# Optimization experiments

Measured on AMD Instinct MI355X. Metric: run time of the kernel, lower is better.

The kernel has to match this reference:

```python
import jax, jax.numpy as jnp
import numpy as np

B, TXT_T, MEL_T, N_MEL = 32, 256, 1600, 40
PAD_MAG = 1.0e12


def setup_inputs() -> dict:
    key = jax.random.key(0)
    k1, k2, k3, k4 = jax.random.split(key, 4)
    mu_logvar = jax.random.normal(k1, (B, TXT_T, 2 * N_MEL), jnp.float32)
    z = jax.random.normal(k2, (B, N_MEL, MEL_T), jnp.float32)
    text_lengths = jax.random.randint(k3, (B,), TXT_T // 2, TXT_T + 1).astype(jnp.int32)
    mel_lengths = jax.random.randint(k4, (B,), MEL_T // 2, MEL_T + 1).astype(jnp.int32)
    return {"mu_logvar": mu_logvar, "z": z,
            "text_lengths": text_lengths, "mel_lengths": mel_lengths}


def _mdn_log_prob(mu_logvar, z):
    # mu_logvar: [B, L, 2C], z: [B, C, T] -> log_prob_matrix [B, L, T]
    C = z.shape[1]
    mu, logvar = jnp.split(mu_logvar, 2, axis=-1)          # [B, L, C] each
    invvar = jnp.exp(-logvar)                               # [B, L, C]
    # mean_c((z - mu)^2 * invvar) expanded via matmuls (no [B,L,T,C] tensor)
    t1 = jnp.einsum('bct,blc->blt', z * z, invvar)
    t2 = jnp.einsum('bct,blc->blt', z, mu * invvar)
    t3 = jnp.sum(mu * mu * invvar, axis=-1)[:, :, None]
    mse = t1 - 2.0 * t2 + t3                                # [B, L, T]
    return -0.5 * (mse / C + jnp.mean(logvar, axis=-1)[:, :, None])


def _forward_dp(lp):
    # forward algorithm: log_alpha over (txt position, mel time) via scan over T
    Bb, L, T = lp.shape
    alpha0 = jnp.full((Bb, L + 1), -PAD_MAG, lp.dtype).at[:, 1].set(lp[:, 0, 0])

    def step(alpha, lp_t):
        stay = alpha[:, 1:] + 1e-7
        go = alpha[:, :-1] + 1e-7
        new = jnp.logaddexp(stay, go) + lp_t                # [B, L]
        alpha_new = jnp.concatenate(
            [jnp.full((Bb, 1), -PAD_MAG, lp.dtype), new], axis=1)
        return alpha_new, new

    _, ys = jax.lax.scan(step, alpha0, jnp.moveaxis(lp[:, :, 1:], 2, 0))
    log_alpha = jnp.concatenate([alpha0[:, 1:][None], ys], axis=0)  # [T, B, L]
    return log_alpha


def _viterbi(lp, text_lengths, mel_lengths):
    Bb, L, T = lp.shape
    beta0 = jnp.full((Bb, L), -PAD_MAG, lp.dtype).at[:, 0].set(lp[:, 0, 0])

    def fstep(beta, lp_t):
        shifted = jnp.concatenate(
            [jnp.full((Bb, 1), -PAD_MAG, lp.dtype), beta[:, :-1]], axis=1)
        new = jnp.maximum(beta, shifted) + lp_t
        return new, new

    _, ys = jax.lax.scan(fstep, beta0, jnp.moveaxis(lp[:, :, 1:], 2, 0))
    log_beta = jnp.transpose(jnp.concatenate([beta0[None], ys], axis=0), (1, 2, 0))  # [B, L, T]

    b_idx = jnp.arange(Bb)
    r0 = (text_lengths - 1).astype(jnp.float32)
    c0 = (mel_lengths - 1).astype(jnp.float32)

    def bstep(carry, _):
        rows, cols = carry
        ri = rows.astype(jnp.int32)
        ci = cols.astype(jnp.int32)
        # torch negative indexing wraps -> emulate with mod
        val_go = log_beta[b_idx, (ri - 1) % L, (ci - 1) % T]
        val_stay = log_beta[b_idx, ri % L, (ci - 1) % T]
        is_go = (val_go > val_stay).astype(rows.dtype)
        new_rows = jax.nn.relu(rows - is_go + 1.0) - 1.0
        new_cols = jax.nn.relu(cols) - 1.0
        return (new_rows, new_cols), new_rows

    _, path_ys = jax.lax.scan(bstep, (r0, c0), None, length=T - 1)
    full = jnp.concatenate([r0[None], path_ys], axis=0)     # [T, B], backward order
    path = full[::-1].T                                     # [B, T], chronological
    align = jax.nn.one_hot(path.astype(jnp.int32), L, dtype=lp.dtype)  # [B, T, L]

    def shift(a, ml):
        # F.pad(..., (-pad, pad)) on time axis: shift valid region to the front
        rolled = jnp.roll(a, -(T - ml), axis=0)
        mask = (jnp.arange(T) < ml)[:, None].astype(a.dtype)
        return rolled * mask

    return jax.vmap(shift)(align, mel_lengths)              # [B, T, L]


def reference(mu_logvar, z, text_lengths, mel_lengths):
    lp = _mdn_log_prob(mu_logvar, z)                        # [B, L, T]
    log_alpha = _forward_dp(lp)                             # [T, B, L]
    b_idx = jnp.arange(lp.shape[0])
    alpha_last = log_alpha[mel_lengths - 1, b_idx, text_lengths - 1]
    mdn_loss = -(alpha_last / mel_lengths.astype(alpha_last.dtype))  # [B]
    alignment = _viterbi(lp, text_lengths, mel_lengths)     # [B, T, L]
    return mdn_loss, alignment, lp
```

## Files before the change

### kernel.cpp

```cpp
#include <hip/hip_runtime.h>
#include <cstdint>
#include <math.h>

#define BB   32
#define LLEN 256
#define TLEN 1600
#define NC   40
#define NEGPADF (-1.0e12f)
#define NEGPADD (-1.0e12)

#define LOG2E_F 1.4426950408889634f
#define LN2_F   0.6931471805599453f
#define C7F     1.4426950408889634e-7f
#define PA_F 1.4426950f
#define PB_F (-0.6484000f)
#define PC_F 0.2057000f

#define OFF_ALIGN 32
#define OFF_LP    (32 + (size_t)BB * TLEN * LLEN)

#define WSB_A    0
#define WSB_KC   (WSB_A + (size_t)BB * LLEN * 80 * 8)
#define WSB_LPT  (WSB_KC + (size_t)BB * LLEN * 8)

__device__ __forceinline__ int imin(int a, int b) { return a < b ? a : b; }

#define WAIT_LGKM0 0xC07F
#define WAIT_VM0   0x3F70

__device__ __forceinline__ int rot1_i32(int x) {
  return __builtin_amdgcn_mov_dpp(x, 0x13C , 0xF, 0xF, true);
}
__device__ __forceinline__ float rot1_f32(float x) {
  return __int_as_float(rot1_i32(__float_as_int(x)));
}
__device__ __forceinline__ double rot1_f64(double x) {
  long long v = __double_as_longlong(x);
  int lo = rot1_i32((int)(v & 0xffffffffLL));
  int hi = rot1_i32((int)(v >> 32));
  return __longlong_as_double(((long long)hi << 32) | (unsigned long long)(unsigned int)lo);
}

__global__ __launch_bounds__(256) void prep_kernel(
    const float* __restrict__ mu_logvar, double* __restrict__ A, double* __restrict__ Kc) {
  int row = blockIdx.x * 4 + (threadIdx.x >> 6);
  int lane = threadIdx.x & 63;
  const float* src = mu_logvar + (size_t)row * (2 * NC);
  double mu = 0.0, lv = 0.0, iv = 0.0, part = 0.0;
  if (lane < NC) {
    mu = (double)src[lane];
    lv = (double)src[NC + lane];
    iv = exp(-lv);
    part = mu * mu * iv + lv;
  }
  for (int m = 1; m < 64; m <<= 1) part += __shfl_xor(part, m, 64);
  const double s = -0.5 / (double)NC;
  if (lane < NC) {
    A[(size_t)row * 80 + lane]      = s * iv;
    A[(size_t)row * 80 + NC + lane] = (1.0 / (double)NC) * mu * iv;
  }
  if (lane == 0) Kc[row] = s * part;
}

__global__ __launch_bounds__(128) void lp_kernel(
    const float* __restrict__ z, const double* __restrict__ A,
    const double* __restrict__ Kc, float* out,
    float* __restrict__ lpTh) {
  int b  = blockIdx.z;
  int l0 = blockIdx.y * 32;
  int t0 = blockIdx.x * 128;
  int tid = threadIdx.x;
  int t = t0 + tid;
  int tv = imin(t, TLEN - 1);
  bool act = (t < TLEN);

  float* lp_out = out + OFF_LP;
  double2* bufA = (double2*)lpTh;
  double2* bufB = (double2*)(out + OFF_ALIGN);

  float zr[NC];
  const float* zb = z + (size_t)b * NC * TLEN;
  #pragma unroll
  for (int c = 0; c < NC; ++c) zr[c] = zb[(size_t)c * TLEN + tv];

  __shared__ __align__(16) double tile[128][17];
  const double* Ab = A + ((size_t)b * LLEN + l0) * 80;
  const double* Kb = Kc + (size_t)b * LLEN + l0;

  for (int g = 0; g < 2; ++g) {
    for (int j16 = 0; j16 < 16; ++j16) {
      int j = g * 16 + j16;
      const double* Ar = Ab + (size_t)j * 80;
      double a0 = Kb[j], a1 = 0.0, a2 = 0.0, a3 = 0.0;
      #pragma unroll
      for (int c = 0; c < NC; c += 2) {
        double z0 = (double)zr[c], z1 = (double)zr[c + 1];
        a0 = fma(Ar[c],          z0 * z0, a0);
        a1 = fma(Ar[NC + c],     z0,      a1);
        a2 = fma(Ar[c + 1],      z1 * z1, a2);
        a3 = fma(Ar[NC + c + 1], z1,      a3);
      }
      double accd = (a0 + a2) + (a1 + a3);
      if (act) lp_out[((size_t)b * LLEN + l0 + j) * TLEN + t] = (float)accd;
      tile[tid][j16] = accd;
    }
    __syncthreads();
    #pragma unroll
    for (int p = 0; p < 4; ++p) {
      int idx = p * 128 + tid;
      int r = idx >> 2, c4 = idx & 3;
      int tr = t0 + r;
      if (tr < TLEN) {
        size_t chunk = ((size_t)b * TLEN + tr) * 64 + (l0 + g * 16) / 4 + c4;
        double2 dA, dB;
        dA.x = tile[r][c4 * 4 + 0]; dA.y = tile[r][c4 * 4 + 1];
        dB.x = tile[r][c4 * 4 + 2]; dB.y = tile[r][c4 * 4 + 3];
        bufA[chunk] = dA;
        bufB[chunk] = dB;
      }
    }
    __syncthreads();
  }
}

__global__ __launch_bounds__(64, 1) void dp_kernel(
    const float* __restrict__ lpTh, const float* outR,
    const int* __restrict__ tlen, const int* __restrict__ mlen,
    float* out) {
  int bid = blockIdx.x;
  bool is_beta = (bid >= BB);
  int b = is_beta ? bid - BB : bid;
  int lane = threadIdx.x & 63;
  int tl = tlen[b];
  int ml = mlen[b];
  const double2* pA = (const double2*)lpTh + (size_t)b * TLEN * 64;
  const double2* pB = (const double2*)(outR + OFF_ALIGN) + (size_t)b * TLEN * 64;
  float* al = out + OFF_ALIGN + (size_t)b * TLEN * LLEN;

  __shared__ uint32_t Dbits[LLEN][TLEN / 32];
  __shared__ int pathL[TLEN];

  if (!is_beta) {
    const float* gB = outR + OFF_LP + (size_t)b * LLEN * TLEN;
    int off2 = (4 * lane + 2) * TLEN;
    int off3 = off2 + TLEN;
    double2 v00 = pA[lane];
    float lp00 = (float)v00.x * LOG2E_F;
    float o0 = (lane == 0) ? lp00 : NEGPADF;
    float o1 = NEGPADF, o2 = NEGPADF, o3 = NEGPADF;
    float f0 = o0, f1 = o1, f2 = o2, f3 = o3;
    float qv = rot1_f32(o3);
    double2 hA0, hA1, hA2, hA3, hA4, hA5, hA6, hA7;
    float r20, r21, r22, r23, r24, r25, r26, r27;
    float r30, r31, r32, r33, r34, r35, r36, r37;
    hA0 = pA[1 * 64 + lane]; { const float* bt = gB + 1; r20 = bt[off2]; r30 = bt[off3]; }
    hA1 = pA[2 * 64 + lane]; { const float* bt = gB + 2; r21 = bt[off2]; r31 = bt[off3]; }
    hA2 = pA[3 * 64 + lane]; { const float* bt = gB + 3; r22 = bt[off2]; r32 = bt[off3]; }
    hA3 = pA[4 * 64 + lane]; { const float* bt = gB + 4; r23 = bt[off2]; r33 = bt[off3]; }
    hA4 = pA[5 * 64 + lane]; { const float* bt = gB + 5; r24 = bt[off2]; r34 = bt[off3]; }
    hA5 = pA[6 * 64 + lane]; { const float* bt = gB + 6; r25 = bt[off2]; r35 = bt[off3]; }
    hA6 = pA[7 * 64 + lane]; { const float* bt = gB + 7; r26 = bt[off2]; r36 = bt[off3]; }
    hA7 = pA[8 * 64 + lane]; { const float* bt = gB + 8; r27 = bt[off2]; r37 = bt[off3]; }
    int t = 1;
    auto stepA = [&](double2& ha, float& r2, float& r3) {
      float v0 = (float)ha.x, v1 = (float)ha.y;
      float v2 = r2, v3 = r3;
      int c = imin(t + 8, TLEN - 1);
      ha = (pA + (size_t)c * 64)[lane];
      { const float* bt = gB + c; r2 = bt[off2]; r3 = bt[off3]; }
      float l0 = fmaf(v0, LOG2E_F, C7F);
      float l1 = fmaf(v1, LOG2E_F, C7F);
      float l2 = fmaf(v2, LOG2E_F, C7F);
      float l3 = fmaf(v3, LOG2E_F, C7F);
      float p = (lane == 0) ? NEGPADF : qv;
      float m0 = fmaxf(o0, p),  d0 = fabsf(o0 - p);
      float m1 = fmaxf(o1, o0), d1 = fabsf(o1 - o0);
      float m2 = fmaxf(o2, o1), d2 = fabsf(o2 - o1);
      float m3 = fmaxf(o3, o2), d3 = fabsf(o3 - o2);
      float y0 = __builtin_amdgcn_exp2f(-d0);
      float y1 = __builtin_amdgcn_exp2f(-d1);
      float y2 = __builtin_amdgcn_exp2f(-d2);
      float y3 = __builtin_amdgcn_exp2f(-d3);
      float s0 = y0 * fmaf(y0, fmaf(y0, PC_F, PB_F), PA_F);
      float s1 = y1 * fmaf(y1, fmaf(y1, PC_F, PB_F), PA_F);
      float s2 = y2 * fmaf(y2, fmaf(y2, PC_F, PB_F), PA_F);
      float s3 = y3 * fmaf(y3, fmaf(y3, PC_F, PB_F), PA_F);
      float n0 = m0 + s0 + l0;
      float n1 = m1 + s1 + l1;
      float n2 = m2 + s2 + l2;
      float n3 = m3 + s3 + l3;
      o0 = n0; o1 = n1; o2 = n2; o3 = n3;
      qv = rot1_f32(o3);
      if (t == ml - 1) { f0 = o0; f1 = o1; f2 = o2; f3 = o3; }
      ++t;
    };
    for (int tb = 0; tb < TLEN / 8; ++tb) {
      stepA(hA0, r20, r30); stepA(hA1, r21, r31);
      stepA(hA2, r22, r32); stepA(hA3, r23, r33);
      stepA(hA4, r24, r34); stepA(hA5, r25, r35);
      stepA(hA6, r26, r36); stepA(hA7, r27, r37);
    }
    int fr = tl - 1;
    if (lane == (fr >> 2)) {
      int sx = fr & 3;
      float val = (sx == 0) ? f0 : (sx == 1) ? f1 : (sx == 2) ? f2 : f3;
      out[b] = -val * LN2_F / (float)ml;
    }
    return;
  }

  float4 z4 = make_float4(0.f, 0.f, 0.f, 0.f);
  double2 v00 = pA[lane];
  double lp00 = v00.x;
  double o0 = (lane == 0) ? lp00 : NEGPADD;
  double o1 = NEGPADD, o2 = NEGPADD, o3 = NEGPADD;
  uint32_t a0 = 0, a1 = (lane == 0) ? 1u : 0u, a2 = 0, a3 = 0;
  double qv = rot1_f64(o3);
  double2 hA0 = pA[1 * 64 + lane], hB0 = pB[1 * 64 + lane];
  double2 hA1 = pA[2 * 64 + lane], hB1 = pB[2 * 64 + lane];
  double2 hA2 = pA[3 * 64 + lane], hB2 = pB[3 * 64 + lane];
  double2 hA3 = pA[4 * 64 + lane], hB3 = pB[4 * 64 + lane];
  double2 hA4 = pA[5 * 64 + lane], hB4 = pB[5 * 64 + lane];
  double2 hA5 = pA[6 * 64 + lane], hB5 = pB[6 * 64 + lane];
  double2 hA6 = pA[7 * 64 + lane], hB6 = pB[7 * 64 + lane];
  double2 hA7 = pA[8 * 64 + lane], hB7 = pB[8 * 64 + lane];
  int t = 1;
  auto stepB = [&](double2& ha, double2& hb) {
    double l0 = ha.x, l1 = ha.y, l2 = hb.x, l3 = hb.y;
    int c = imin(t + 8, TLEN - 1);
    ha = (pA + (size_t)c * 64)[lane];
    hb = (pB + (size_t)c * 64)[lane];
    double p = (lane == 0) ? NEGPADD : qv;
    double n0 = fmax(o0, p)  + l0;
    double n1 = fmax(o1, o0) + l1;
    double n2 = fmax(o2, o1) + l2;
    double n3 = fmax(o3, o2) + l3;
    qv = rot1_f64(n3);
    asm("v_cmp_gt_f64 vcc, %1, %2\n\t"
        "v_addc_co_u32 %0, vcc, %0, %0, vcc"
        : "+v"(a0) : "v"(qv), "v"(n0) : "vcc");
    asm("v_cmp_gt_f64 vcc, %1, %2\n\t"
        "v_addc_co_u32 %0, vcc, %0, %0, vcc"
        : "+v"(a1) : "v"(n0), "v"(n1) : "vcc");
    asm("v_cmp_gt_f64 vcc, %1, %2\n\t"
        "v_addc_co_u32 %0, vcc, %0, %0, vcc"
        : "+v"(a2) : "v"(n1), "v"(n2) : "vcc");
    asm("v_cmp_gt_f64 vcc, %1, %2\n\t"
        "v_addc_co_u32 %0, vcc, %0, %0, vcc"
        : "+v"(a3) : "v"(n2), "v"(n3) : "vcc");
    o0 = n0; o1 = n1; o2 = n2; o3 = n3;
    if ((t & 31) == 31) {
      int wd = t >> 5;
      Dbits[4 * lane + 0][wd] = a0; a0 = 0;
      Dbits[4 * lane + 1][wd] = a1; a1 = 0;
      Dbits[4 * lane + 2][wd] = a2; a2 = 0;
      Dbits[4 * lane + 3][wd] = a3; a3 = 0;
    }
    if (t > 8) ((float4*)(al + (size_t)(t - 8) * LLEN))[lane] = z4;
    ++t;
  };
  for (int tb = 0; tb < TLEN / 8; ++tb) {
    stepB(hA0, hB0); stepB(hA1, hB1); stepB(hA2, hB2); stepB(hA3, hB3);
    stepB(hA4, hB4); stepB(hA5, hB5); stepB(hA6, hB6); stepB(hA7, hB7);
  }
  ((float4*)al)[lane] = z4;
  #pragma unroll
  for (int c = TLEN - 7; c < TLEN; ++c)
    ((float4*)(al + (size_t)c * LLEN))[lane] = z4;

  __builtin_amdgcn_s_waitcnt(WAIT_LGKM0);

  if (lane == 0) {
    int r = tl - 1;
    pathL[ml - 1] = r;
    int curR = 1 << 30, curW = -1;
    uint32_t W = 0;
    for (int qq = ml - 2; qq >= 0; --qq) {
      int w2 = qq >> 5;
      if (r >= 0 && (r != curR || w2 != curW)) { W = Dbits[r][w2]; curR = r; curW = w2; }
      int g = (r >= 0) ? (int)((W >> (31 - (qq & 31))) & 1u) : 0;
      r -= g;
      pathL[qq] = r;
    }
  }
  __builtin_amdgcn_s_waitcnt(WAIT_LGKM0);
  __builtin_amdgcn_s_waitcnt(WAIT_VM0);

  for (int tt = lane; tt < ml; tt += 64) {
    int p = pathL[tt];
    if (p >= 0) al[(size_t)tt * LLEN + p] = 1.0f;
  }
}

extern "C" void kernel_launch(void* const* d_in, const int* in_sizes, int n_in,
                              void* d_out, int out_size, void* d_ws, size_t ws_size,
                              hipStream_t stream) {
  const float* mu_logvar = (const float*)d_in[0];
  const float* z         = (const float*)d_in[1];
  const int*   tlv       = (const int*)d_in[2];
  const int*   mlv       = (const int*)d_in[3];
  float* out = (float*)d_out;
  char*  wsb = (char*)d_ws;

  double* Ad   = (double*)(wsb + WSB_A);
  double* Kcd  = (double*)(wsb + WSB_KC);
  float*  lpTh = (float*)(wsb + WSB_LPT);

  prep_kernel<<<dim3(BB * LLEN / 4), 256, 0, stream>>>(mu_logvar, Ad, Kcd);
  lp_kernel<<<dim3(13, 8, BB), 128, 0, stream>>>(z, Ad, Kcd, out, lpTh);
  dp_kernel<<<dim3(2 * BB), 64, 0, stream>>>(lpTh, out, tlv, mlv, out);
}
```

Measured before the change: 527.3 us.

## Split DP across two wavefronts with wavefront-skewed pipelining and separate finalize kernel

The forward and Viterbi DP are split so that each block uses two wavefronts, each owning half of the text positions (2 per lane instead of 4). The second wavefront lags the first by one 32-step chunk and reads boundary values through shared memory, with a barrier after each chunk. The lp buffer layout changes so each wavefront reads a contiguous half, and alignment zeroing plus path scatter move into a new, widely parallel finalize kernel. This shortens the per-step serial dependency chain and takes the alignment-store traffic off the latency-bound DP. The cost is per-chunk barriers, a two-chunk pipeline fill, and an extra kernel launch.

```diff
diff --git a/kernel.cpp b/kernel.cpp
--- a/kernel.cpp
+++ b/kernel.cpp
@@ -16,17 +16,26 @@
 #define PB_F (-0.6484000f)
 #define PC_F 0.2057000f
 
+#define NCHUNK (TLEN / 32)
+#define NITER  (NCHUNK + 2)
+
 #define OFF_ALIGN 32
 #define OFF_LP    (32 + (size_t)BB * TLEN * LLEN)
 
 #define WSB_A    0
 #define WSB_KC   (WSB_A + (size_t)BB * LLEN * 80 * 8)
 #define WSB_LPT  (WSB_KC + (size_t)BB * LLEN * 8)
+#define WSB_PATH (WSB_LPT + (size_t)BB * TLEN * 64 * 16)
 
 __device__ __forceinline__ int imin(int a, int b) { return a < b ? a : b; }
 
 #define WAIT_LGKM0 0xC07F
-#define WAIT_VM0   0x3F70
+
+__device__ __forceinline__ void bar() {
+  asm volatile("" ::: "memory");
+  __builtin_amdgcn_s_barrier();
+  asm volatile("" ::: "memory");
+}
 
 __device__ __forceinline__ int rot1_i32(int x) {
   return __builtin_amdgcn_mov_dpp(x, 0x13C , 0xF, 0xF, true);
@@ -105,172 +114,240 @@
       tile[tid][j16] = accd;
     }
     __syncthreads();
-    #pragma unroll
-    for (int p = 0; p < 4; ++p) {
-      int idx = p * 128 + tid;
-      int r = idx >> 2, c4 = idx & 3;
-      int tr = t0 + r;
-      if (tr < TLEN) {
-        size_t chunk = ((size_t)b * TLEN + tr) * 64 + (l0 + g * 16) / 4 + c4;
-        double2 dA, dB;
-        dA.x = tile[r][c4 * 4 + 0]; dA.y = tile[r][c4 * 4 + 1];
-        dB.x = tile[r][c4 * 4 + 2]; dB.y = tile[r][c4 * 4 + 3];
-        bufA[chunk] = dA;
-        bufB[chunk] = dB;
+    {
+      bool toB = (l0 + g * 16) >= 128;
+      double2* dst = toB ? bufB : bufA;
+      int slotbase = (l0 + g * 16) / 2 - (toB ? 64 : 0);
+      #pragma unroll
+      for (int p8 = 0; p8 < 8; ++p8) {
+        int idx = p8 * 128 + tid;
+        int r = idx >> 3, s = idx & 7;
+        int tr = t0 + r;
+        if (tr < TLEN) {
+          double2 d;
+          d.x = tile[r][2 * s];
+          d.y = tile[r][2 * s + 1];
+          dst[((size_t)b * TLEN + tr) * 64 + slotbase + s] = d;
+        }
       }
     }
     __syncthreads();
   }
 }
 
-__global__ __launch_bounds__(64, 1) void dp_kernel(
+__global__ __launch_bounds__(128, 1) void dp_kernel(
     const float* __restrict__ lpTh, const float* outR,
     const int* __restrict__ tlen, const int* __restrict__ mlen,
-    float* out) {
+    float* out, int* __restrict__ pathg) {
   int bid = blockIdx.x;
   bool is_beta = (bid >= BB);
   int b = is_beta ? bid - BB : bid;
-  int lane = threadIdx.x & 63;
+  int tid = threadIdx.x;
+  int lane = tid & 63;
+  int wv = tid >> 6;
   int tl = tlen[b];
   int ml = mlen[b];
   const double2* pA = (const double2*)lpTh + (size_t)b * TLEN * 64;
   const double2* pB = (const double2*)(outR + OFF_ALIGN) + (size_t)b * TLEN * 64;
-  float* al = out + OFF_ALIGN + (size_t)b * TLEN * LLEN;
 
   __shared__ uint32_t Dbits[LLEN][TLEN / 32];
   __shared__ int pathL[TLEN];
+  __shared__ double2 bndP[1616];
+  float* bndF = (float*)bndP;
+
+  const double2* myd = wv ? pB : pA;
+
+  if (tid == 0) {
+    if (is_beta) { bndP[0].x = NEGPADD; bndP[0].y = pA[0].x; }
+    else         { bndF[0] = NEGPADF; }
+  }
+  __syncthreads();
+
+  double2 D0 = myd[1 * 64 + lane], D1 = myd[2 * 64 + lane];
+  double2 D2 = myd[3 * 64 + lane], D3 = myd[4 * 64 + lane];
+  double2 D4 = myd[5 * 64 + lane], D5 = myd[6 * 64 + lane];
+  double2 D6 = myd[7 * 64 + lane], D7 = myd[8 * 64 + lane];
 
   if (!is_beta) {
-    const float* gB = outR + OFF_LP + (size_t)b * LLEN * TLEN;
-    int off2 = (4 * lane + 2) * TLEN;
-    int off3 = off2 + TLEN;
-    double2 v00 = pA[lane];
-    float lp00 = (float)v00.x * LOG2E_F;
-    float o0 = (lane == 0) ? lp00 : NEGPADF;
-    float o1 = NEGPADF, o2 = NEGPADF, o3 = NEGPADF;
-    float f0 = o0, f1 = o1, f2 = o2, f3 = o3;
-    float qv = rot1_f32(o3);
-    double2 hA0, hA1, hA2, hA3, hA4, hA5, hA6, hA7;
-    float r20, r21, r22, r23, r24, r25, r26, r27;
-    float r30, r31, r32, r33, r34, r35, r36, r37;
-    hA0 = pA[1 * 64 + lane]; { const float* bt = gB + 1; r20 = bt[off2]; r30 = bt[off3]; }
-    hA1 = pA[2 * 64 + lane]; { const float* bt = gB + 2; r21 = bt[off2]; r31 = bt[off3]; }
-    hA2 = pA[3 * 64 + lane]; { const float* bt = gB + 3; r22 = bt[off2]; r32 = bt[off3]; }
-    hA3 = pA[4 * 64 + lane]; { const float* bt = gB + 4; r23 = bt[off2]; r33 = bt[off3]; }
-    hA4 = pA[5 * 64 + lane]; { const float* bt = gB + 5; r24 = bt[off2]; r34 = bt[off3]; }
-    hA5 = pA[6 * 64 + lane]; { const float* bt = gB + 6; r25 = bt[off2]; r35 = bt[off3]; }
-    hA6 = pA[7 * 64 + lane]; { const float* bt = gB + 7; r26 = bt[off2]; r36 = bt[off3]; }
-    hA7 = pA[8 * 64 + lane]; { const float* bt = gB + 8; r27 = bt[off2]; r37 = bt[off3]; }
+    float lp00 = (float)pA[0].x * LOG2E_F;
+    float o0 = (wv == 0 && lane == 0) ? lp00 : NEGPADF;
+    float o1 = NEGPADF;
+    float f0 = o0, f1 = o1;
+    float qv = rot1_f32(o1);
+    float bcar = 0.f, bq0 = 0.f, bq1 = 0.f, bq2 = 0.f, bq3 = 0.f;
+    float bq4 = 0.f, bq5 = 0.f, bq6 = 0.f, bq7 = 0.f;
     int t = 1;
-    auto stepA = [&](double2& ha, float& r2, float& r3) {
-      float v0 = (float)ha.x, v1 = (float)ha.y;
-      float v2 = r2, v3 = r3;
+    auto stepL = [&](double2& D) {
+      float v0 = (float)D.x, v1 = (float)D.y;
       int c = imin(t + 8, TLEN - 1);
-      ha = (pA + (size_t)c * 64)[lane];
-      { const float* bt = gB + c; r2 = bt[off2]; r3 = bt[off3]; }
+      D = myd[(size_t)c * 64 + lane];
       float l0 = fmaf(v0, LOG2E_F, C7F);
       float l1 = fmaf(v1, LOG2E_F, C7F);
-      float l2 = fmaf(v2, LOG2E_F, C7F);
-      float l3 = fmaf(v3, LOG2E_F, C7F);
       float p = (lane == 0) ? NEGPADF : qv;
       float m0 = fmaxf(o0, p),  d0 = fabsf(o0 - p);
       float m1 = fmaxf(o1, o0), d1 = fabsf(o1 - o0);
-      float m2 = fmaxf(o2, o1), d2 = fabsf(o2 - o1);
-      float m3 = fmaxf(o3, o2), d3 = fabsf(o3 - o2);
       float y0 = __builtin_amdgcn_exp2f(-d0);
       float y1 = __builtin_amdgcn_exp2f(-d1);
-      float y2 = __builtin_amdgcn_exp2f(-d2);
-      float y3 = __builtin_amdgcn_exp2f(-d3);
       float s0 = y0 * fmaf(y0, fmaf(y0, PC_F, PB_F), PA_F);
       float s1 = y1 * fmaf(y1, fmaf(y1, PC_F, PB_F), PA_F);
-      float s2 = y2 * fmaf(y2, fmaf(y2, PC_F, PB_F), PA_F);
-      float s3 = y3 * fmaf(y3, fmaf(y3, PC_F, PB_F), PA_F);
-      float n0 = m0 + s0 + l0;
-      float n1 = m1 + s1 + l1;
-      float n2 = m2 + s2 + l2;
-      float n3 = m3 + s3 + l3;
-      o0 = n0; o1 = n1; o2 = n2; o3 = n3;
-      qv = rot1_f32(o3);
-      if (t == ml - 1) { f0 = o0; f1 = o1; f2 = o2; f3 = o3; }
+      o0 = m0 + s0 + l0;
+      o1 = m1 + s1 + l1;
+      qv = rot1_f32(o1);
+      if (lane == 63) bndF[t] = o1;
+      if (t == ml - 1) { f0 = o0; f1 = o1; }
       ++t;
     };
-    for (int tb = 0; tb < TLEN / 8; ++tb) {
-      stepA(hA0, r20, r30); stepA(hA1, r21, r31);
-      stepA(hA2, r22, r32); stepA(hA3, r23, r33);
-      stepA(hA4, r24, r34); stepA(hA5, r25, r35);
-      stepA(hA6, r26, r36); stepA(hA7, r27, r37);
+    auto stepF = [&](double2& D, float& bq) {
+      float v0 = (float)D.x, v1 = (float)D.y;
+      int c = imin(t + 8, TLEN - 1);
+      D = myd[(size_t)c * 64 + lane];
+      float bc = bq;
+      bq = bndF[t + 8];
+      float l0 = fmaf(v0, LOG2E_F, C7F);
+      float l1 = fmaf(v1, LOG2E_F, C7F);
+      float p = (lane == 0) ? bcar : qv;
+      float m0 = fmaxf(o0, p),  d0 = fabsf(o0 - p);
+      float m1 = fmaxf(o1, o0), d1 = fabsf(o1 - o0);
+      float y0 = __builtin_amdgcn_exp2f(-d0);
+      float y1 = __builtin_amdgcn_exp2f(-d1);
+      float s0 = y0 * fmaf(y0, fmaf(y0, PC_F, PB_F), PA_F);
+      float s1 = y1 * fmaf(y1, fmaf(y1, PC_F, PB_F), PA_F);
+      o0 = m0 + s0 + l0;
+      o1 = m1 + s1 + l1;
+      qv = rot1_f32(o1);
+      bcar = bc;
+      if (t == ml - 1) { f0 = o0; f1 = o1; }
+      ++t;
+    };
+    for (int k = 0; k < NITER; ++k) {
+      if (wv == 0) {
+        if (k < NCHUNK) {
+          #pragma unroll 1
+          for (int u = 0; u < 4; ++u) {
+            stepL(D0); stepL(D1); stepL(D2); stepL(D3);
+            stepL(D4); stepL(D5); stepL(D6); stepL(D7);
+          }
+          __builtin_amdgcn_s_waitcnt(WAIT_LGKM0);
+        }
+      } else {
+        if (k == 1) {
+          bcar = bndF[0];
+          bq0 = bndF[1]; bq1 = bndF[2]; bq2 = bndF[3]; bq3 = bndF[4];
+          bq4 = bndF[5]; bq5 = bndF[6]; bq6 = bndF[7]; bq7 = bndF[8];
+        }
+        if (k >= 2) {
+          #pragma unroll 1
+          for (int u = 0; u < 4; ++u) {
+            stepF(D0, bq0); stepF(D1, bq1); stepF(D2, bq2); stepF(D3, bq3);
+            stepF(D4, bq4); stepF(D5, bq5); stepF(D6, bq6); stepF(D7, bq7);
+          }
+        }
+      }
+      bar();
     }
     int fr = tl - 1;
-    if (lane == (fr >> 2)) {
-      int sx = fr & 3;
-      float val = (sx == 0) ? f0 : (sx == 1) ? f1 : (sx == 2) ? f2 : f3;
+    if ((fr >> 7) == wv && lane == ((fr & 127) >> 1)) {
+      float val = (fr & 1) ? f1 : f0;
       out[b] = -val * LN2_F / (float)ml;
     }
     return;
   }
 
-  float4 z4 = make_float4(0.f, 0.f, 0.f, 0.f);
-  double2 v00 = pA[lane];
-  double lp00 = v00.x;
-  double o0 = (lane == 0) ? lp00 : NEGPADD;
-  double o1 = NEGPADD, o2 = NEGPADD, o3 = NEGPADD;
-  uint32_t a0 = 0, a1 = (lane == 0) ? 1u : 0u, a2 = 0, a3 = 0;
-  double qv = rot1_f64(o3);
-  double2 hA0 = pA[1 * 64 + lane], hB0 = pB[1 * 64 + lane];
-  double2 hA1 = pA[2 * 64 + lane], hB1 = pB[2 * 64 + lane];
-  double2 hA2 = pA[3 * 64 + lane], hB2 = pB[3 * 64 + lane];
-  double2 hA3 = pA[4 * 64 + lane], hB3 = pB[4 * 64 + lane];
-  double2 hA4 = pA[5 * 64 + lane], hB4 = pB[5 * 64 + lane];
-  double2 hA5 = pA[6 * 64 + lane], hB5 = pB[6 * 64 + lane];
-  double2 hA6 = pA[7 * 64 + lane], hB6 = pB[7 * 64 + lane];
-  double2 hA7 = pA[8 * 64 + lane], hB7 = pB[8 * 64 + lane];
-  int t = 1;
-  auto stepB = [&](double2& ha, double2& hb) {
-    double l0 = ha.x, l1 = ha.y, l2 = hb.x, l3 = hb.y;
-    int c = imin(t + 8, TLEN - 1);
-    ha = (pA + (size_t)c * 64)[lane];
-    hb = (pB + (size_t)c * 64)[lane];
-    double p = (lane == 0) ? NEGPADD : qv;
-    double n0 = fmax(o0, p)  + l0;
-    double n1 = fmax(o1, o0) + l1;
-    double n2 = fmax(o2, o1) + l2;
-    double n3 = fmax(o3, o2) + l3;
-    qv = rot1_f64(n3);
-    asm("v_cmp_gt_f64 vcc, %1, %2\n\t"
-        "v_addc_co_u32 %0, vcc, %0, %0, vcc"
-        : "+v"(a0) : "v"(qv), "v"(n0) : "vcc");
-    asm("v_cmp_gt_f64 vcc, %1, %2\n\t"
-        "v_addc_co_u32 %0, vcc, %0, %0, vcc"
-        : "+v"(a1) : "v"(n0), "v"(n1) : "vcc");
-    asm("v_cmp_gt_f64 vcc, %1, %2\n\t"
-        "v_addc_co_u32 %0, vcc, %0, %0, vcc"
-        : "+v"(a2) : "v"(n1), "v"(n2) : "vcc");
-    asm("v_cmp_gt_f64 vcc, %1, %2\n\t"
-        "v_addc_co_u32 %0, vcc, %0, %0, vcc"
-        : "+v"(a3) : "v"(n2), "v"(n3) : "vcc");
-    o0 = n0; o1 = n1; o2 = n2; o3 = n3;
-    if ((t & 31) == 31) {
-      int wd = t >> 5;
-      Dbits[4 * lane + 0][wd] = a0; a0 = 0;
-      Dbits[4 * lane + 1][wd] = a1; a1 = 0;
-      Dbits[4 * lane + 2][wd] = a2; a2 = 0;
-      Dbits[4 * lane + 3][wd] = a3; a3 = 0;
-    }
-    if (t > 8) ((float4*)(al + (size_t)(t - 8) * LLEN))[lane] = z4;
-    ++t;
-  };
-  for (int tb = 0; tb < TLEN / 8; ++tb) {
-    stepB(hA0, hB0); stepB(hA1, hB1); stepB(hA2, hB2); stepB(hA3, hB3);
-    stepB(hA4, hB4); stepB(hA5, hB5); stepB(hA6, hB6); stepB(hA7, hB7);
-  }
-  ((float4*)al)[lane] = z4;
-  #pragma unroll
-  for (int c = TLEN - 7; c < TLEN; ++c)
-    ((float4*)(al + (size_t)c * LLEN))[lane] = z4;
-
-  __builtin_amdgcn_s_waitcnt(WAIT_LGKM0);
-
-  if (lane == 0) {
+  {
+    double lp00 = pA[0].x;
+    double o0 = (wv == 0 && lane == 0) ? lp00 : NEGPADD;
+    double o1 = NEGPADD;
+    uint32_t a0 = 0, a1 = (wv == 0 && lane == 0) ? 1u : 0u, aW = 0;
+    double qv = rot1_f64(o1);
+    double bcar = 0.0;
+    double2 bq0, bq1, bq2, bq3, bq4, bq5, bq6, bq7;
+    bq0 = bq1 = bq2 = bq3 = bq4 = bq5 = bq6 = bq7 = make_double2(0.0, 0.0);
+    int t = 1;
+    auto stepLb = [&](double2& D) {
+      double l0 = D.x, l1 = D.y;
+      int c = imin(t + 8, TLEN - 1);
+      D = myd[(size_t)c * 64 + lane];
+      double p = (lane == 0) ? NEGPADD : qv;
+      double n0 = fmax(o0, p)  + l0;
+      double n1 = fmax(o1, o0) + l1;
+      qv = rot1_f64(n1);
+      asm("v_cmp_gt_f64 vcc, %1, %2\n\t"
+          "v_addc_co_u32 %0, vcc, %0, %0, vcc"
+          : "+v"(a0) : "v"(qv), "v"(n0) : "vcc");
+      asm("v_cmp_gt_f64 vcc, %1, %2\n\t"
+          "v_addc_co_u32 %0, vcc, %0, %0, vcc"
+          : "+v"(a1) : "v"(n0), "v"(n1) : "vcc");
+      o0 = n0; o1 = n1;
+      if (lane == 63) bndP[t].x = n1;
+      if (lane == 0)  bndP[t].y = n0;
+      if ((t & 31) == 31) {
+        int wd = t >> 5;
+        if (lane != 0) Dbits[2 * lane][wd] = a0;
+        Dbits[2 * lane + 1][wd] = a1;
+        a0 = 0; a1 = 0;
+      }
+      ++t;
+    };
+    auto stepFb = [&](double2& D, double2& bq) {
+      double l0 = D.x, l1 = D.y;
+      int c = imin(t + 8, TLEN - 1);
+      D = myd[(size_t)c * 64 + lane];
+      double2 bc = bq;
+      bq = bndP[t + 8];
+      double p = (lane == 0) ? bcar : qv;
+      double n0 = fmax(o0, p)  + l0;
+      double n1 = fmax(o1, o0) + l1;
+      qv = rot1_f64(n1);
+      double bx = (lane == 0) ? bc.x : qv;
+      asm("v_cmp_gt_f64 vcc, %1, %2\n\t"
+          "v_addc_co_u32 %0, vcc, %0, %0, vcc"
+          : "+v"(a0) : "v"(bx), "v"(n0) : "vcc");
+      asm("v_cmp_gt_f64 vcc, %1, %2\n\t"
+          "v_addc_co_u32 %0, vcc, %0, %0, vcc"
+          : "+v"(a1) : "v"(n0), "v"(n1) : "vcc");
+      asm("v_cmp_gt_f64 vcc, %1, %2\n\t"
+          "v_addc_co_u32 %0, vcc, %0, %0, vcc"
+          : "+v"(aW) : "v"(n1), "v"(bc.y) : "vcc");
+      o0 = n0; o1 = n1; bcar = bc.x;
+      if ((t & 31) == 31) {
+        int wd = t >> 5;
+        Dbits[128 + 2 * lane][wd] = a0;
+        Dbits[129 + 2 * lane][wd] = a1;
+        if (lane == 63) Dbits[0][wd] = aW;
+        a0 = 0; a1 = 0; aW = 0;
+      }
+      ++t;
+    };
+    for (int k = 0; k < NITER; ++k) {
+      if (wv == 0) {
+        if (k < NCHUNK) {
+          #pragma unroll 1
+          for (int u = 0; u < 4; ++u) {
+            stepLb(D0); stepLb(D1); stepLb(D2); stepLb(D3);
+            stepLb(D4); stepLb(D5); stepLb(D6); stepLb(D7);
+          }
+          __builtin_amdgcn_s_waitcnt(WAIT_LGKM0);
+        }
+      } else {
+        if (k == 1) {
+          bcar = bndP[0].x;
+          bq0 = bndP[1]; bq1 = bndP[2]; bq2 = bndP[3]; bq3 = bndP[4];
+          bq4 = bndP[5]; bq5 = bndP[6]; bq6 = bndP[7]; bq7 = bndP[8];
+        }
+        if (k >= 2) {
+          #pragma unroll 1
+          for (int u = 0; u < 4; ++u) {
+            stepFb(D0, bq0); stepFb(D1, bq1); stepFb(D2, bq2); stepFb(D3, bq3);
+            stepFb(D4, bq4); stepFb(D5, bq5); stepFb(D6, bq6); stepFb(D7, bq7);
+          }
+        }
+      }
+      bar();
+    }
+  }
+  __syncthreads();
+
+  if (tid == 0) {
     int r = tl - 1;
     pathL[ml - 1] = r;
     int curR = 1 << 30, curW = -1;
@@ -283,12 +360,31 @@
       pathL[qq] = r;
     }
   }
-  __builtin_amdgcn_s_waitcnt(WAIT_LGKM0);
-  __builtin_amdgcn_s_waitcnt(WAIT_VM0);
-
-  for (int tt = lane; tt < ml; tt += 64) {
-    int p = pathL[tt];
-    if (p >= 0) al[(size_t)tt * LLEN + p] = 1.0f;
+  __syncthreads();
+  for (int tt = tid; tt < ml; tt += 128) pathg[b * TLEN + tt] = pathL[tt];
+}
+
+__global__ __launch_bounds__(256) void finalize_kernel(
+    const int* __restrict__ mlen, const int* __restrict__ pathg,
+    float* __restrict__ out) {
+  int b = blockIdx.y;
+  int t0 = blockIdx.x * 8;
+  float* al = out + OFF_ALIGN + (size_t)b * TLEN * LLEN;
+  float4 z4 = make_float4(0.f, 0.f, 0.f, 0.f);
+  #pragma unroll
+  for (int p = 0; p < 2; ++p) {
+    int idx = p * 256 + threadIdx.x;
+    int r = idx >> 6, c4 = idx & 63;
+    *(float4*)(al + (size_t)(t0 + r) * LLEN + c4 * 4) = z4;
+  }
+  __syncthreads();
+  if (threadIdx.x < 8) {
+    int t = t0 + threadIdx.x;
+    int ml = mlen[b];
+    if (t < ml) {
+      int p = pathg[b * TLEN + t];
+      if (p >= 0) al[(size_t)t * LLEN + p] = 1.0f;
+    }
   }
 }
 
@@ -305,8 +401,10 @@
   double* Ad   = (double*)(wsb + WSB_A);
   double* Kcd  = (double*)(wsb + WSB_KC);
   float*  lpTh = (float*)(wsb + WSB_LPT);
+  int*    path = (int*)(wsb + WSB_PATH);
 
   prep_kernel<<<dim3(BB * LLEN / 4), 256, 0, stream>>>(mu_logvar, Ad, Kcd);
   lp_kernel<<<dim3(13, 8, BB), 128, 0, stream>>>(z, Ad, Kcd, out, lpTh);
-  dp_kernel<<<dim3(2 * BB), 64, 0, stream>>>(lpTh, out, tlv, mlv, out);
-}
+  dp_kernel<<<dim3(2 * BB), 128, 0, stream>>>(lpTh, out, tlv, mlv, out, path);
+  finalize_kernel<<<dim3(TLEN / 8, BB), 256, 0, stream>>>(mlv, path, out);
+}
```

Result: slower. 580.1 us (+10.0%).
